# Optimization experiments

Measured on AMD Instinct MI355X. Metric: run time of the kernel, lower is better.

Reference implementation:

```python
import jax, jax.numpy as jnp
import numpy as np
from jax import lax

BATCH, T, S, E = 32, 2048, 512, 32  # batch, seq_len, n_states, alphabet


def setup_inputs() -> dict:
    key = jax.random.key(0)
    k1, k2, k3, k4 = jax.random.split(key, 4)
    # one-hot observation sequences [B, T, E]
    obs = jax.random.randint(k1, (BATCH, T), 0, E)
    inputs = jax.nn.one_hot(obs, E, dtype=jnp.float32)
    # row-stochastic transition matrix A [S, S]
    A = jax.nn.softmax(jax.random.normal(k2, (S, S), dtype=jnp.float32), axis=-1)
    # row-stochastic emission matrix B [S, E]
    Bem = jax.nn.softmax(jax.random.normal(k3, (S, E), dtype=jnp.float32), axis=-1)
    # initial state distribution pi [S]
    pi = jax.nn.softmax(jax.random.normal(k4, (S,), dtype=jnp.float32))
    return {"inputs": inputs, "A": A, "Bem": Bem, "pi": pi}


def reference(inputs, A, Bem, pi):
    # HMM forward algorithm with per-step scaling (sum-normalization),
    # accumulating log-likelihood: loglik += log(sum_s alpha_t[s]).
    # inputs: [B, T, E] one-hot; A: [S, S]; Bem: [S, E]; pi: [S]
    x = jnp.swapaxes(inputs, 0, 1)                 # [T, B, E]
    em = jnp.einsum('tbe,se->tbs', x, Bem)         # emission probs per step [T, B, S]

    alpha0 = pi[None, :] * em[0]                   # [B, S]
    z0 = jnp.sum(alpha0, axis=-1, keepdims=True)   # [B, 1]
    alpha0 = alpha0 / z0
    loglik0 = jnp.log(z0[:, 0])                    # [B]

    def step(carry, em_t):
        alpha, loglik = carry
        a = (alpha @ A) * em_t                     # [B, S]
        z = jnp.sum(a, axis=-1, keepdims=True)
        return (a / z, loglik + jnp.log(z[:, 0])), None

    (alpha, loglik), _ = lax.scan(step, (alpha0, loglik0), em[1:])
    return loglik                                  # loglik_state [B]
```

## Files before the change

kernel.cpp:

```cpp
#include <hip/hip_runtime.h>
#include <math.h>


#define BATCH 32
#define T_LEN 2048
#define S_N   512
#define E_N   32
#define CHUNKS 256
#define L_CH  (T_LEN / CHUNKS)
#define WARM  2
#define WIN   (L_CH + WARM)
#define ASTRIDE 520
#define SA 256.0f
#define SM 128.0f

typedef __attribute__((ext_vector_type(16))) float floatx16;
typedef __attribute__((ext_vector_type(4))) short short4v;
typedef long long i64;

__device__ __forceinline__ float bf16_to_f(short s) {
    unsigned int u = ((unsigned int)(unsigned short)s) << 16;
    return __builtin_bit_cast(float, u);
}
__device__ __forceinline__ short f_to_bf16(float f) {
    unsigned int u = __builtin_bit_cast(unsigned int, f);
    u = (u + 0x7FFFu + ((u >> 16) & 1u)) >> 16;
    return (short)u;
}

__global__ __launch_bounds__(256) void prep_kernel(
    const float* __restrict__ A, const float* __restrict__ Bem,
    i64* __restrict__ Aperm, short* __restrict__ emTg, float* __restrict__ out)
{
    __shared__ float s_A[16 * 512];
    const int g = blockIdx.x, tid = threadIdx.x;
    if (g < 32) {
        const float* src = A + (size_t)g * 16 * 512;
#pragma unroll
        for (int p = 0; p < 8; ++p) {
            int idx = tid + 256 * p;
            *(float4*)&s_A[idx * 4] = *(const float4*)(src + idx * 4);
        }
        __syncthreads();
        const int lane_o = tid & 63;
        const int h = lane_o >> 5, mm = lane_o & 31;
#pragma unroll
        for (int p = 0; p < 4; ++p) {
            int tile = (tid >> 6) + 4 * p;
            int n = tile * 32 + mm;
            float f[8];
#pragma unroll
            for (int j = 0; j < 8; ++j)
                f[j] = s_A[(h * 8 + j) * 512 + n] * SM;
            int lo = __builtin_amdgcn_cvt_pk_fp8_f32(f[0], f[1], 0, 0);
            lo     = __builtin_amdgcn_cvt_pk_fp8_f32(f[2], f[3], lo, 1);
            int hi = __builtin_amdgcn_cvt_pk_fp8_f32(f[4], f[5], 0, 0);
            hi     = __builtin_amdgcn_cvt_pk_fp8_f32(f[6], f[7], hi, 1);
            Aperm[(size_t)(tile * 32 + g) * 64 + lane_o] =
                (i64)(unsigned int)lo | ((i64)(unsigned int)hi << 32);
        }
    } else {
        int base = (g - 32) * 512;
#pragma unroll
        for (int p = 0; p < 2; ++p) {
            int idx = base + tid + 256 * p;
            int e = idx >> 9, n = idx & 511;
            emTg[idx] = f_to_bf16(Bem[n * E_N + e]);
        }
        if (g == 32 && tid < 32) out[tid] = 0.0f;
    }
}


__global__ __launch_bounds__(1024, 4) void hmm_kernel(
    const float* __restrict__ inputs, const i64* __restrict__ Aperm,
    const float* __restrict__ pi, const short* __restrict__ emTg,
    float* __restrict__ out)
{
    __shared__ i64   s_alpha8[BATCH * ASTRIDE / 8];
    __shared__ float s_part[16][32];
    __shared__ float s_zi[32];
    __shared__ int   s_obs[BATCH * WIN];
    unsigned char* s_alpha = (unsigned char*)s_alpha8;

    const int c    = blockIdx.x;
    const int tid  = threadIdx.x;
    const int wv   = tid >> 6;
    const int lane = tid & 63;
    const int h    = lane >> 5;
    const int m    = lane & 31;

    const int t_log = c * L_CH;
    const int t_end = t_log + L_CH;
    const int t_w0  = t_end - WIN;
    int t0 = t_log - 1 - WARM;
    const bool exact0 = (t0 < 0);
    const int t_begin = (t0 < 0 ? 0 : t0) + 1;

    if (tid < BATCH * WIN) {
        int mm = tid / WIN, tt = tid - mm * WIN;
        int t = t_w0 + tt;
        if (t >= 0) {
            const float* p = inputs + ((size_t)mm * T_LEN + t) * E_N;
            float o = 0.0f;
#pragma unroll
            for (int gg = 0; gg < 8; ++gg) {
                float4 v = *(const float4*)(p + gg * 4);
                o += (4 * gg) * v.x + (4 * gg + 1) * v.y + (4 * gg + 2) * v.z + (4 * gg + 3) * v.w;
            }
            s_obs[tid] = (int)(o + 0.5f);
        }
    }
    __syncthreads();

    float logacc = 0.0f;
    float zprod  = 1.0f;

    if (exact0) {
        if (tid < 512) {
            const int dt0 = -t_w0;
            float pj = pi[tid];
            for (int mm = 0; mm < 32; ++mm) {
                int o = s_obs[mm * WIN + dt0];
                float v = pj * bf16_to_f(emTg[o * S_N + tid]);
                v += __shfl_xor(v, 1);  v += __shfl_xor(v, 2);  v += __shfl_xor(v, 4);
                v += __shfl_xor(v, 8);  v += __shfl_xor(v, 16); v += __shfl_xor(v, 32);
                if (lane == 0) s_part[wv][mm] = v;
            }
        }
        __syncthreads();
        if (tid < 32) {
            float z = 0.0f;
#pragma unroll
            for (int w2 = 0; w2 < 8; ++w2) z += s_part[w2][tid];
            logacc += logf(z);
            s_zi[tid] = SA / z;
        }
        __syncthreads();
        if (tid < 512) {
            const int dt0 = -t_w0;
            float pj = pi[tid];
            for (int mm = 0; mm < 32; ++mm) {
                int o = s_obs[mm * WIN + dt0];
                float v = pj * bf16_to_f(emTg[o * S_N + tid]) * s_zi[mm];
                s_alpha[mm * ASTRIDE + tid] =
                    (unsigned char)(__builtin_amdgcn_cvt_pk_fp8_f32(v, 0.0f, 0, 0) & 0xff);
            }
        }
        __syncthreads();
    } else {
        const i64 u8 = 0x3030303030303030LL;
        for (int i = tid; i < BATCH * ASTRIDE / 8; i += 1024) s_alpha8[i] = u8;
        __syncthreads();
    }

    i64 areg[32];
#pragma unroll
    for (int i = 0; i < 32; ++i)
        areg[i] = Aperm[(size_t)(wv * 32 + i) * 64 + lane];

    for (int t = t_begin; t < t_end; ++t) {
        const int dtw = t - t_w0;
        const int o = s_obs[m * WIN + dtw];
        const short* emp = emTg + o * S_N + wv * 32 + h * 4;
        short4v emv[4];
#pragma unroll
        for (int gg = 0; gg < 4; ++gg)
            emv[gg] = *(const short4v*)(emp + gg * 8);

        floatx16 acc = (floatx16)(0.0f);
#pragma unroll
        for (int ks = 0; ks < 32; ++ks) {
            i64 b = *(const i64*)(s_alpha + m * ASTRIDE + ks * 16 + h * 8);
            acc = __builtin_amdgcn_mfma_f32_32x32x16_fp8_fp8(areg[ks], b, acc, 0, 0, 0);
        }

        float psum = 0.0f;
#pragma unroll
        for (int reg = 0; reg < 16; ++reg) {
            float v = acc[reg] * bf16_to_f(emv[reg >> 2][reg & 3]);
            acc[reg] = v;
            psum += v;
        }
        psum += __shfl_xor(psum, 32);
        if (lane < 32) s_part[wv][m] = psum;
        __syncthreads();

        float zin = 0.0f;
#pragma unroll
        for (int w2 = 0; w2 < 16; ++w2) zin += s_part[w2][m];
        if (t >= t_log) zprod *= zin * 0x1p-15f;
        float zi = SA / zin;

#pragma unroll
        for (int gg = 0; gg < 4; ++gg) {
            int pk = __builtin_amdgcn_cvt_pk_fp8_f32(acc[gg * 4] * zi, acc[gg * 4 + 1] * zi, 0, 0);
            pk     = __builtin_amdgcn_cvt_pk_fp8_f32(acc[gg * 4 + 2] * zi, acc[gg * 4 + 3] * zi, pk, 1);
            *(int*)(s_alpha + m * ASTRIDE + wv * 32 + gg * 8 + h * 4) = pk;
        }
        __syncthreads();
    }

    if (tid < 32) atomicAdd(out + tid, logacc + logf(zprod));
}


extern "C" void kernel_launch(void* const* d_in, const int* in_sizes, int n_in,
                              void* d_out, int out_size, void* d_ws, size_t ws_size,
                              hipStream_t stream) {
    const float* inputs = (const float*)d_in[0];
    const float* A      = (const float*)d_in[1];
    const float* Bem    = (const float*)d_in[2];
    const float* pi     = (const float*)d_in[3];
    float* out = (float*)d_out;

    i64*   Aperm = (i64*)d_ws;
    short* emTg  = (short*)((char*)d_ws + 256 * 1024);

    prep_kernel<<<64, 256, 0, stream>>>(A, Bem, Aperm, emTg, out);
    hmm_kernel<<<CHUNKS, 1024, 0, stream>>>(inputs, Aperm, pi, emTg, out);
}
```

Baseline: 105.3 us.

## Double-buffer alpha and partial sums to remove one barrier per step

The recurrence now ping-pongs between two copies of the fp8 alpha buffer and the per-wave partial sums. Normalization is deferred by one step: each step reads the previous step's partial sums to form the scale factor and folds it into the emission multiply, then writes unscaled fp8 alpha directly. This cuts the two __syncthreads per timestep down to one and lets the normalizer reduction overlap the MFMA chain. In exchange it uses twice the LDS for alpha and needs extra bookkeeping for the initial and final normalizers, which risks subtle off-by-one errors in the log-likelihood accumulation.

```diff
diff --git a/kernel.cpp b/kernel.cpp
--- a/kernel.cpp
+++ b/kernel.cpp
@@ -77,11 +77,10 @@
     const float* __restrict__ pi, const short* __restrict__ emTg,
     float* __restrict__ out)
 {
-    __shared__ i64   s_alpha8[BATCH * ASTRIDE / 8];
-    __shared__ float s_part[16][32];
+    __shared__ i64   s_alpha8[2][BATCH * ASTRIDE / 8];
+    __shared__ float s_part[2][16][32];
     __shared__ float s_zi[32];
     __shared__ int   s_obs[BATCH * WIN];
-    unsigned char* s_alpha = (unsigned char*)s_alpha8;
 
     const int c    = blockIdx.x;
     const int tid  = threadIdx.x;
@@ -96,6 +95,7 @@
     int t0 = t_log - 1 - WARM;
     const bool exact0 = (t0 < 0);
     const int t_begin = (t0 < 0 ? 0 : t0) + 1;
+    const int pb0 = t_begin & 1;
 
     if (tid < BATCH * WIN) {
         int mm = tid / WIN, tt = tid - mm * WIN;
@@ -111,12 +111,18 @@
             s_obs[tid] = (int)(o + 0.5f);
         }
     }
+    if (tid < 512) (&s_part[pb0][0][0])[tid] = SA / 16.0f;
+    if (!exact0) {
+        const i64 u8 = 0x3030303030303030LL;
+        for (int i = tid; i < BATCH * ASTRIDE / 8; i += 1024) s_alpha8[pb0][i] = u8;
+    }
     __syncthreads();
 
     float logacc = 0.0f;
     float zprod  = 1.0f;
 
     if (exact0) {
+        unsigned char* sA0 = (unsigned char*)s_alpha8[pb0];
         if (tid < 512) {
             const int dt0 = -t_w0;
             float pj = pi[tid];
@@ -125,14 +131,14 @@
                 float v = pj * bf16_to_f(emTg[o * S_N + tid]);
                 v += __shfl_xor(v, 1);  v += __shfl_xor(v, 2);  v += __shfl_xor(v, 4);
                 v += __shfl_xor(v, 8);  v += __shfl_xor(v, 16); v += __shfl_xor(v, 32);
-                if (lane == 0) s_part[wv][mm] = v;
+                if (lane == 0) s_part[1 ^ pb0][wv][mm] = v;
             }
         }
         __syncthreads();
         if (tid < 32) {
             float z = 0.0f;
 #pragma unroll
-            for (int w2 = 0; w2 < 8; ++w2) z += s_part[w2][tid];
+            for (int w2 = 0; w2 < 8; ++w2) z += s_part[1 ^ pb0][w2][tid];
             logacc += logf(z);
             s_zi[tid] = SA / z;
         }
@@ -143,15 +149,11 @@
             for (int mm = 0; mm < 32; ++mm) {
                 int o = s_obs[mm * WIN + dt0];
                 float v = pj * bf16_to_f(emTg[o * S_N + tid]) * s_zi[mm];
-                s_alpha[mm * ASTRIDE + tid] =
+                sA0[mm * ASTRIDE + tid] =
                     (unsigned char)(__builtin_amdgcn_cvt_pk_fp8_f32(v, 0.0f, 0, 0) & 0xff);
             }
         }
         __syncthreads();
-    } else {
-        const i64 u8 = 0x3030303030303030LL;
-        for (int i = tid; i < BATCH * ASTRIDE / 8; i += 1024) s_alpha8[i] = u8;
-        __syncthreads();
     }
 
     i64 areg[32];
@@ -160,6 +162,10 @@
         areg[i] = Aperm[(size_t)(wv * 32 + i) * 64 + lane];
 
     for (int t = t_begin; t < t_end; ++t) {
+        const int p = t & 1;
+        const unsigned char* aR = (const unsigned char*)s_alpha8[p];
+        unsigned char*       aW = (unsigned char*)s_alpha8[1 ^ p];
+
         const int dtw = t - t_w0;
         const int o = s_obs[m * WIN + dtw];
         const short* emp = emTg + o * S_N + wv * 32 + h * 4;
@@ -168,37 +174,44 @@
         for (int gg = 0; gg < 4; ++gg)
             emv[gg] = *(const short4v*)(emp + gg * 8);
 
+        float zin = 0.0f;
+#pragma unroll
+        for (int w2 = 0; w2 < 16; ++w2) zin += s_part[p][w2][m];
+
         floatx16 acc = (floatx16)(0.0f);
 #pragma unroll
         for (int ks = 0; ks < 32; ++ks) {
-            i64 b = *(const i64*)(s_alpha + m * ASTRIDE + ks * 16 + h * 8);
+            i64 b = *(const i64*)(aR + m * ASTRIDE + ks * 16 + h * 8);
             acc = __builtin_amdgcn_mfma_f32_32x32x16_fp8_fp8(areg[ks], b, acc, 0, 0, 0);
         }
 
+        if (t > t_log && t > t_begin) zprod *= zin * 0x1p-15f;
+        const float f = SA / zin;
+
         float psum = 0.0f;
 #pragma unroll
         for (int reg = 0; reg < 16; ++reg) {
-            float v = acc[reg] * bf16_to_f(emv[reg >> 2][reg & 3]);
+            float v = acc[reg] * bf16_to_f(emv[reg >> 2][reg & 3]) * f;
             acc[reg] = v;
             psum += v;
         }
         psum += __shfl_xor(psum, 32);
-        if (lane < 32) s_part[wv][m] = psum;
-        __syncthreads();
-
+        if (lane < 32) s_part[1 ^ p][wv][m] = psum;
+
+#pragma unroll
+        for (int gg = 0; gg < 4; ++gg) {
+            int pk = __builtin_amdgcn_cvt_pk_fp8_f32(acc[gg * 4], acc[gg * 4 + 1], 0, 0);
+            pk     = __builtin_amdgcn_cvt_pk_fp8_f32(acc[gg * 4 + 2], acc[gg * 4 + 3], pk, 1);
+            *(int*)(aW + m * ASTRIDE + wv * 32 + gg * 8 + h * 4) = pk;
+        }
+        __syncthreads();
+    }
+
+    {
         float zin = 0.0f;
 #pragma unroll
-        for (int w2 = 0; w2 < 16; ++w2) zin += s_part[w2][m];
-        if (t >= t_log) zprod *= zin * 0x1p-15f;
-        float zi = SA / zin;
-
-#pragma unroll
-        for (int gg = 0; gg < 4; ++gg) {
-            int pk = __builtin_amdgcn_cvt_pk_fp8_f32(acc[gg * 4] * zi, acc[gg * 4 + 1] * zi, 0, 0);
-            pk     = __builtin_amdgcn_cvt_pk_fp8_f32(acc[gg * 4 + 2] * zi, acc[gg * 4 + 3] * zi, pk, 1);
-            *(int*)(s_alpha + m * ASTRIDE + wv * 32 + gg * 8 + h * 4) = pk;
-        }
-        __syncthreads();
+        for (int w2 = 0; w2 < 16; ++w2) zin += s_part[t_end & 1][w2][m];
+        zprod *= zin * 0x1p-15f;
     }
 
     if (tid < 32) atomicAdd(out + tid, logacc + logf(zprod));
```

Result: faster. 100.7 us (-4.4%).
